# Kernel optimization log

Measured on AMD Instinct MI355X. Metric: run time of the kernel, lower is better.

The kernel has to match this reference:

```python
import jax, jax.numpy as jnp
import numpy as np

D_IN = 768
D_OUT = 768
SEQ = 2048
BATCH = 4


def setup_inputs() -> dict:
    key = jax.random.key(0)
    kx, kq, kk, kv = jax.random.split(key, 4)
    # torch Linear weight shape: [d_out, d_in]; default init ~ U(-1/sqrt(d_in), 1/sqrt(d_in))
    bound = 1.0 / np.sqrt(D_IN)
    x = jax.random.normal(kx, (BATCH, SEQ, D_IN), dtype=jnp.float32)
    Wq = jax.random.uniform(kq, (D_OUT, D_IN), jnp.float32, -bound, bound)
    Wk = jax.random.uniform(kk, (D_OUT, D_IN), jnp.float32, -bound, bound)
    Wv = jax.random.uniform(kv, (D_OUT, D_IN), jnp.float32, -bound, bound)
    return {"x": x, "Wq": Wq, "Wk": Wk, "Wv": Wv}


def reference(x, Wq, Wk, Wv):
    # QKV projections (no bias): x [b, n, d_in] @ W.T -> [b, n, d_out]
    q = jnp.einsum("bnd,od->bno", x, Wq)
    k = jnp.einsum("bnd,od->bno", x, Wk)
    v = jnp.einsum("bnd,od->bno", x, Wv)
    n = x.shape[1]
    d_k = k.shape[-1]
    # scores [b, n, n]; causal mask: positions j > i set to -inf
    scores = jnp.einsum("bqd,bkd->bqk", q, k)
    causal = jnp.triu(jnp.ones((n, n), dtype=bool), k=1)  # True above diagonal
    scores = jnp.where(causal[None, :, :], -jnp.inf, scores)
    attn = jax.nn.softmax(scores / jnp.sqrt(jnp.asarray(d_k, scores.dtype)), axis=-1)
    # dropout p=0.0 -> identity
    context = jnp.einsum("bqk,bkd->bqd", attn, v)
    return context
```

## Files before the change

### kernel.cpp

```cpp
#include <hip/hip_runtime.h>
#include <hip/hip_bf16.h>

typedef float f32x4 __attribute__((ext_vector_type(4)));
typedef short s16x8 __attribute__((ext_vector_type(8)));

#define B_ 4
#define S_ 2048
#define D_ 768

typedef const __attribute__((address_space(1))) char* gas_t;
typedef __attribute__((address_space(3))) char* las_t;

__device__ __forceinline__ void gload_lds16(const void* g, void* l) {
  __builtin_amdgcn_global_load_lds((gas_t)g, (las_t)l, 16, 0, 0);
}

__global__ void cvt_kernel(const float* __restrict__ x,
                           const float* __restrict__ wq,
                           const float* __restrict__ wk,
                           const float* __restrict__ wv,
                           __hip_bfloat16* __restrict__ xb,
                           __hip_bfloat16* __restrict__ wqb,
                           __hip_bfloat16* __restrict__ wkb,
                           __hip_bfloat16* __restrict__ wvb) {
  const int NX = B_ * S_ * D_ / 4;
  const int NW = D_ * D_ / 4;
  int stride = gridDim.x * blockDim.x;
  for (int j = blockIdx.x * blockDim.x + threadIdx.x; j < NX + 3 * NW; j += stride) {
    const float4* src; __hip_bfloat16* dst; int off;
    if (j < NX)             { src = (const float4*)x;  dst = xb;  off = j; }
    else if (j < NX + NW)   { src = (const float4*)wq; dst = wqb; off = j - NX; }
    else if (j < NX + 2*NW) { src = (const float4*)wk; dst = wkb; off = j - NX - NW; }
    else                    { src = (const float4*)wv; dst = wvb; off = j - NX - 2*NW; }
    float4 v = src[off];
    dst[4*off+0] = __float2bfloat16(v.x);
    dst[4*off+1] = __float2bfloat16(v.y);
    dst[4*off+2] = __float2bfloat16(v.z);
    dst[4*off+3] = __float2bfloat16(v.w);
  }
}

__device__ __forceinline__ void stage_tile64(const __hip_bfloat16* __restrict__ base,
                                             size_t stride, int r0, int k0,
                                             char* lds, int w, int l) {
#pragma unroll
  for (int it = 0; it < 4; ++it) {
    int ra = it * 32 + w * 8 + (l >> 3);
    int slot = (l & 7) ^ ((l >> 3) & 7);
    gload_lds16(base + (size_t)(r0 + ra) * stride + k0 + slot * 8,
                lds + it * 4096 + w * 1024);
  }
}

#define SWZ_IDX(R, s) ((R) * 64 + (((s) ^ ((R) & 7)) * 8))

__launch_bounds__(256, 2)
__global__ void qkv_gemm(const __hip_bfloat16* __restrict__ xb,
                         const __hip_bfloat16* __restrict__ wqb,
                         const __hip_bfloat16* __restrict__ wkb,
                         const __hip_bfloat16* __restrict__ wvb,
                         __hip_bfloat16* __restrict__ Qb,
                         __hip_bfloat16* __restrict__ Kb,
                         __hip_bfloat16* __restrict__ Vt) {
  __shared__ __hip_bfloat16 At[2][128 * 64];
  __shared__ __hip_bfloat16 Bt[2][128 * 64];
  const int z = blockIdx.z;
  const __hip_bfloat16* Ag;
  const __hip_bfloat16* Bg;
  int m0, n0;
  if (z == 0)      { Ag = xb;  Bg = wqb; m0 = blockIdx.x * 128; n0 = blockIdx.y * 128; }
  else if (z == 1) { Ag = xb;  Bg = wkb; m0 = blockIdx.x * 128; n0 = blockIdx.y * 128; }
  else             { Ag = wvb; Bg = xb;  m0 = blockIdx.y * 128; n0 = blockIdx.x * 128; }

  const int tid = threadIdx.x, w = tid >> 6, l = tid & 63;
  const int wr = w >> 1, wc = w & 1;
  f32x4 acc[4][4] = {};

  stage_tile64(Ag, 768, m0, 0, (char*)At[0], w, l);
  stage_tile64(Bg, 768, n0, 0, (char*)Bt[0], w, l);
  int cur = 0;
  for (int k0 = 0; k0 < 768; k0 += 64) {
    __syncthreads();
    if (k0 + 64 < 768) {
      stage_tile64(Ag, 768, m0, k0 + 64, (char*)At[cur ^ 1], w, l);
      stage_tile64(Bg, 768, n0, k0 + 64, (char*)Bt[cur ^ 1], w, l);
    }
#pragma unroll
    for (int kk = 0; kk < 2; ++kk) {
      s16x8 a[4], b[4];
      int s = kk * 4 + (l >> 4);
#pragma unroll
      for (int i = 0; i < 4; ++i) {
        int Ra = wr * 64 + i * 16 + (l & 15);
        int Rb = wc * 64 + i * 16 + (l & 15);
        a[i] = *(const s16x8*)&At[cur][SWZ_IDX(Ra, s)];
        b[i] = *(const s16x8*)&Bt[cur][SWZ_IDX(Rb, s)];
      }
#pragma unroll
      for (int i = 0; i < 4; ++i)
#pragma unroll
        for (int j = 0; j < 4; ++j)
          acc[i][j] = __builtin_amdgcn_mfma_f32_16x16x32_bf16(a[i], b[j], acc[i][j], 0, 0, 0);
    }
    cur ^= 1;
  }

  if (z < 2) {
    __hip_bfloat16* outp = (z == 0) ? Qb : Kb;
#pragma unroll
    for (int i = 0; i < 4; ++i) {
      int m = m0 + wr * 64 + i * 16 + (l >> 4) * 4;
#pragma unroll
      for (int j = 0; j < 4; ++j) {
        int n = n0 + wc * 64 + j * 16 + (l & 15);
#pragma unroll
        for (int r = 0; r < 4; ++r)
          outp[(size_t)(m + r) * 768 + n] = __float2bfloat16(acc[i][j][r]);
      }
    }
  } else {
#pragma unroll
    for (int i = 0; i < 4; ++i) {
      int dd = m0 + wr * 64 + i * 16 + (l >> 4) * 4;
#pragma unroll
      for (int j = 0; j < 4; ++j) {
        int sg = n0 + wc * 64 + j * 16 + (l & 15);
        int bb = sg >> 11, sl = sg & 2047;
#pragma unroll
        for (int r = 0; r < 4; ++r)
          Vt[(size_t)bb * D_ * S_ + (size_t)(dd + r) * S_ + sl] = __float2bfloat16(acc[i][j][r]);
      }
    }
  }
}

__launch_bounds__(256, 2)
__global__ void qk_gemm(const __hip_bfloat16* __restrict__ Qb,
                        const __hip_bfloat16* __restrict__ Kb,
                        __hip_bfloat16* __restrict__ Sb) {
  __shared__ __hip_bfloat16 At[2][128 * 64];
  __shared__ __hip_bfloat16 Bt[2][128 * 64];
  const int qt = blockIdx.x, kt = blockIdx.y, b = blockIdx.z;
  if (kt > qt) return;
  const int m0 = qt * 128, n0 = kt * 128;
  const __hip_bfloat16* Ag = Qb + (size_t)b * S_ * D_;
  const __hip_bfloat16* Bg = Kb + (size_t)b * S_ * D_;
  const int tid = threadIdx.x, w = tid >> 6, l = tid & 63;
  const int wr = w >> 1, wc = w & 1;
  const float SC = 0.03608439182435161f * 1.4426950408889634f;
  f32x4 acc[4][4] = {};

  stage_tile64(Ag, D_, m0, 0, (char*)At[0], w, l);
  stage_tile64(Bg, D_, n0, 0, (char*)Bt[0], w, l);
  int cur = 0;
  for (int k0 = 0; k0 < D_; k0 += 64) {
    __syncthreads();
    if (k0 + 64 < D_) {
      stage_tile64(Ag, D_, m0, k0 + 64, (char*)At[cur ^ 1], w, l);
      stage_tile64(Bg, D_, n0, k0 + 64, (char*)Bt[cur ^ 1], w, l);
    }
#pragma unroll
    for (int kk = 0; kk < 2; ++kk) {
      s16x8 a[4], bfr[4];
      int s = kk * 4 + (l >> 4);
#pragma unroll
      for (int i = 0; i < 4; ++i) {
        int Ra = wr * 64 + i * 16 + (l & 15);
        int Rb = wc * 64 + i * 16 + (l & 15);
        a[i]   = *(const s16x8*)&At[cur][SWZ_IDX(Ra, s)];
        bfr[i] = *(const s16x8*)&Bt[cur][SWZ_IDX(Rb, s)];
      }
#pragma unroll
      for (int i = 0; i < 4; ++i)
#pragma unroll
        for (int j = 0; j < 4; ++j)
          acc[i][j] = __builtin_amdgcn_mfma_f32_16x16x32_bf16(a[i], bfr[j], acc[i][j], 0, 0, 0);
    }
    cur ^= 1;
  }

#pragma unroll
  for (int i = 0; i < 4; ++i) {
    int m = m0 + wr * 64 + i * 16 + (l >> 4) * 4;
#pragma unroll
    for (int j = 0; j < 4; ++j) {
      int n = n0 + wc * 64 + j * 16 + (l & 15);
#pragma unroll
      for (int r = 0; r < 4; ++r) {
        float zz = (n > m + r) ? -1e30f : acc[i][j][r] * SC;
        Sb[(size_t)(b * S_ + m + r) * S_ + n] = __float2bfloat16(zz);
      }
    }
  }
}

__launch_bounds__(256, 4)
__global__ void softmax_kernel(const __hip_bfloat16* __restrict__ Sb,
                               __hip_bfloat16* __restrict__ Pb) {
  const int tid = threadIdx.x, w = tid >> 6, l = tid & 63;
  const int r = blockIdx.x * 4 + w;
  const int q = r & (S_ - 1);
  const int L = ((q >> 7) + 1) << 7;
  const ushort* srow = (const ushort*)(Sb + (size_t)r * S_);
  ushort* prow = (ushort*)(Pb + (size_t)r * S_);
  f32x4 ch[8];
#pragma unroll
  for (int it = 0; it < 8; ++it) {
    int idx = it * 256 + l * 4;
    if (idx < L) {
      ushort4 u = *(const ushort4*)&srow[idx];
      ch[it].x = __uint_as_float((unsigned)u.x << 16);
      ch[it].y = __uint_as_float((unsigned)u.y << 16);
      ch[it].z = __uint_as_float((unsigned)u.z << 16);
      ch[it].w = __uint_as_float((unsigned)u.w << 16);
    } else {
      ch[it].x = -1e30f; ch[it].y = -1e30f; ch[it].z = -1e30f; ch[it].w = -1e30f;
    }
  }
  float mx = -1e30f;
#pragma unroll
  for (int it = 0; it < 8; ++it)
    mx = fmaxf(mx, fmaxf(fmaxf(ch[it].x, ch[it].y), fmaxf(ch[it].z, ch[it].w)));
#pragma unroll
  for (int d = 1; d < 64; d <<= 1) mx = fmaxf(mx, __shfl_xor(mx, d, 64));
  float sum = 0.f;
#pragma unroll
  for (int it = 0; it < 8; ++it) {
    ch[it].x = exp2f(ch[it].x - mx);
    ch[it].y = exp2f(ch[it].y - mx);
    ch[it].z = exp2f(ch[it].z - mx);
    ch[it].w = exp2f(ch[it].w - mx);
    sum += (ch[it].x + ch[it].y) + (ch[it].z + ch[it].w);
  }
#pragma unroll
  for (int d = 1; d < 64; d <<= 1) sum += __shfl_xor(sum, d, 64);
  const float rinv = 1.0f / sum;
#pragma unroll
  for (int it = 0; it < 8; ++it) {
    int idx = it * 256 + l * 4;
    if (idx < L) {
      __hip_bfloat16 h0 = __float2bfloat16(ch[it].x * rinv);
      __hip_bfloat16 h1 = __float2bfloat16(ch[it].y * rinv);
      __hip_bfloat16 h2 = __float2bfloat16(ch[it].z * rinv);
      __hip_bfloat16 h3 = __float2bfloat16(ch[it].w * rinv);
      ushort4 u;
      u.x = *(ushort*)&h0; u.y = *(ushort*)&h1; u.z = *(ushort*)&h2; u.w = *(ushort*)&h3;
      *(ushort4*)&prow[idx] = u;
    }
  }
}

__launch_bounds__(256, 2)
__global__ void pv_gemm(const __hip_bfloat16* __restrict__ Pb,
                        const __hip_bfloat16* __restrict__ Vt,
                        float* __restrict__ out) {
  __shared__ __hip_bfloat16 At[2][128 * 64];
  __shared__ __hip_bfloat16 Bt[2][128 * 64];
  const int qt = 15 - (int)blockIdx.x, dt = blockIdx.y, b = blockIdx.z;
  const int m0 = qt * 128, n0 = dt * 128;
  const __hip_bfloat16* Ag = Pb + (size_t)b * S_ * S_;
  const __hip_bfloat16* Bg = Vt + (size_t)b * D_ * S_;
  const int tid = threadIdx.x, w = tid >> 6, l = tid & 63;
  const int wr = w >> 1, wc = w & 1;
  const int kmax = (qt + 1) * 128;
  f32x4 acc[4][4] = {};

  stage_tile64(Ag, S_, m0, 0, (char*)At[0], w, l);
  stage_tile64(Bg, S_, n0, 0, (char*)Bt[0], w, l);
  int cur = 0;
  for (int k0 = 0; k0 < kmax; k0 += 64) {
    __syncthreads();
    if (k0 + 64 < kmax) {
      stage_tile64(Ag, S_, m0, k0 + 64, (char*)At[cur ^ 1], w, l);
      stage_tile64(Bg, S_, n0, k0 + 64, (char*)Bt[cur ^ 1], w, l);
    }
#pragma unroll
    for (int kk = 0; kk < 2; ++kk) {
      s16x8 a[4], bfr[4];
      int s = kk * 4 + (l >> 4);
#pragma unroll
      for (int i = 0; i < 4; ++i) {
        int Ra = wr * 64 + i * 16 + (l & 15);
        int Rb = wc * 64 + i * 16 + (l & 15);
        a[i]   = *(const s16x8*)&At[cur][SWZ_IDX(Ra, s)];
        bfr[i] = *(const s16x8*)&Bt[cur][SWZ_IDX(Rb, s)];
      }
#pragma unroll
      for (int i = 0; i < 4; ++i)
#pragma unroll
        for (int j = 0; j < 4; ++j)
          acc[i][j] = __builtin_amdgcn_mfma_f32_16x16x32_bf16(a[i], bfr[j], acc[i][j], 0, 0, 0);
    }
    cur ^= 1;
  }

#pragma unroll
  for (int i = 0; i < 4; ++i) {
    int m = m0 + wr * 64 + i * 16 + (l >> 4) * 4;
#pragma unroll
    for (int j = 0; j < 4; ++j) {
      int n = n0 + wc * 64 + j * 16 + (l & 15);
#pragma unroll
      for (int r = 0; r < 4; ++r)
        out[(size_t)(b * S_ + m + r) * D_ + n] = acc[i][j][r];
    }
  }
}

extern "C" void kernel_launch(void* const* d_in, const int* in_sizes, int n_in,
                              void* d_out, int out_size, void* d_ws, size_t ws_size,
                              hipStream_t stream) {
  const float* x  = (const float*)d_in[0];
  const float* wq = (const float*)d_in[1];
  const float* wk = (const float*)d_in[2];
  const float* wv = (const float*)d_in[3];
  char* ws = (char*)d_ws;
  __hip_bfloat16* xb  = (__hip_bfloat16*)(ws + 0);
  __hip_bfloat16* wqb = (__hip_bfloat16*)(ws + 12582912);
  __hip_bfloat16* wkb = (__hip_bfloat16*)(ws + 12582912 + 1179648);
  __hip_bfloat16* wvb = (__hip_bfloat16*)(ws + 12582912 + 2 * 1179648);
  __hip_bfloat16* Qb  = (__hip_bfloat16*)(ws + 16121856);
  __hip_bfloat16* Kb  = (__hip_bfloat16*)(ws + 28704768);
  __hip_bfloat16* Vt  = (__hip_bfloat16*)(ws + 41287680);
  __hip_bfloat16* Sb  = (__hip_bfloat16*)(ws + 53870592);
  __hip_bfloat16* Pb  = (__hip_bfloat16*)(ws + 0);

  cvt_kernel<<<2048, 256, 0, stream>>>(x, wq, wk, wv, xb, wqb, wkb, wvb);
  qkv_gemm<<<dim3(64, 6, 3), 256, 0, stream>>>(xb, wqb, wkb, wvb, Qb, Kb, Vt);
  qk_gemm<<<dim3(16, 16, 4), 256, 0, stream>>>(Qb, Kb, Sb);
  softmax_kernel<<<2048, 256, 0, stream>>>(Sb, Pb);
  pv_gemm<<<dim3(16, 6, 4), 256, 0, stream>>>(Pb, Vt, (float*)d_out);
}
```

Baseline: 196.4 us.

## Use 256x256 tiles for QKV GEMM and split-K the long causal PV rows

The QKV projection GEMM moves to 256x256 tiles with 512 threads, explicit waitcnt/barrier scheduling and raised MFMA priority, so each block reuses more of what it loads. The PV GEMM splits the upper eight query tiles along K into two halves written to fp32 partial buffers, which evens out causal load imbalance across blocks. A new combine kernel then sums the partials into the output. This costs an extra kernel launch and extra fp32 traffic, and the larger QKV tile lowers occupancy and leaves fewer blocks (288).

After: 214.4 us. 1.09x slower.

```diff
diff --git a/kernel.cpp b/kernel.cpp
--- a/kernel.cpp
+++ b/kernel.cpp
@@ -52,83 +52,110 @@
   }
 }
 
+__device__ __forceinline__ void stage_tile256(const __hip_bfloat16* __restrict__ base,
+                                              size_t stride, int r0, int k0,
+                                              char* lds, int w, int l) {
+#pragma unroll
+  for (int it = 0; it < 4; ++it) {
+    int row = it * 64 + w * 8 + (l >> 3);
+    int slot = (l & 7) ^ ((l >> 3) & 7);
+    gload_lds16(base + (size_t)(r0 + row) * stride + k0 + slot * 8,
+                lds + it * 8192 + w * 1024);
+  }
+}
+
 #define SWZ_IDX(R, s) ((R) * 64 + (((s) ^ ((R) & 7)) * 8))
 
-__launch_bounds__(256, 2)
-__global__ void qkv_gemm(const __hip_bfloat16* __restrict__ xb,
-                         const __hip_bfloat16* __restrict__ wqb,
-                         const __hip_bfloat16* __restrict__ wkb,
-                         const __hip_bfloat16* __restrict__ wvb,
-                         __hip_bfloat16* __restrict__ Qb,
-                         __hip_bfloat16* __restrict__ Kb,
-                         __hip_bfloat16* __restrict__ Vt) {
-  __shared__ __hip_bfloat16 At[2][128 * 64];
-  __shared__ __hip_bfloat16 Bt[2][128 * 64];
+__launch_bounds__(512, 1)
+__global__ void qkv_gemm256(const __hip_bfloat16* __restrict__ xb,
+                            const __hip_bfloat16* __restrict__ wqb,
+                            const __hip_bfloat16* __restrict__ wkb,
+                            const __hip_bfloat16* __restrict__ wvb,
+                            __hip_bfloat16* __restrict__ Qb,
+                            __hip_bfloat16* __restrict__ Kb,
+                            __hip_bfloat16* __restrict__ Vt) {
+  __shared__ __hip_bfloat16 At[2][256 * 64];
+  __shared__ __hip_bfloat16 Bt[2][256 * 64];
   const int z = blockIdx.z;
   const __hip_bfloat16* Ag;
   const __hip_bfloat16* Bg;
   int m0, n0;
-  if (z == 0)      { Ag = xb;  Bg = wqb; m0 = blockIdx.x * 128; n0 = blockIdx.y * 128; }
-  else if (z == 1) { Ag = xb;  Bg = wkb; m0 = blockIdx.x * 128; n0 = blockIdx.y * 128; }
-  else             { Ag = wvb; Bg = xb;  m0 = blockIdx.y * 128; n0 = blockIdx.x * 128; }
+  if (z == 0)      { Ag = xb;  Bg = wqb; m0 = blockIdx.x * 256; n0 = blockIdx.y * 256; }
+  else if (z == 1) { Ag = xb;  Bg = wkb; m0 = blockIdx.x * 256; n0 = blockIdx.y * 256; }
+  else             { Ag = wvb; Bg = xb;  m0 = blockIdx.y * 256; n0 = blockIdx.x * 256; }
 
   const int tid = threadIdx.x, w = tid >> 6, l = tid & 63;
-  const int wr = w >> 1, wc = w & 1;
-  f32x4 acc[4][4] = {};
-
-  stage_tile64(Ag, 768, m0, 0, (char*)At[0], w, l);
-  stage_tile64(Bg, 768, n0, 0, (char*)Bt[0], w, l);
-  int cur = 0;
-  for (int k0 = 0; k0 < 768; k0 += 64) {
-    __syncthreads();
-    if (k0 + 64 < 768) {
-      stage_tile64(Ag, 768, m0, k0 + 64, (char*)At[cur ^ 1], w, l);
-      stage_tile64(Bg, 768, n0, k0 + 64, (char*)Bt[cur ^ 1], w, l);
-    }
+  const int wm = w >> 2, wn = w & 3;
+  f32x4 acc[8][4] = {};
+
+  stage_tile256(Ag, 768, m0, 0, (char*)At[0], w, l);
+  stage_tile256(Bg, 768, n0, 0, (char*)Bt[0], w, l);
+
+  const int NT = 12;
+  for (int t = 0; t < NT; ++t) {
+    __builtin_amdgcn_sched_barrier(0);
+    asm volatile("s_waitcnt lgkmcnt(0)" ::: "memory");
+    __builtin_amdgcn_s_barrier();
+    __builtin_amdgcn_sched_barrier(0);
+    if (t + 1 < NT) {
+      stage_tile256(Ag, 768, m0, (t + 1) * 64, (char*)At[(t + 1) & 1], w, l);
+      stage_tile256(Bg, 768, n0, (t + 1) * 64, (char*)Bt[(t + 1) & 1], w, l);
+      asm volatile("s_waitcnt vmcnt(8)" ::: "memory");
+    } else {
+      asm volatile("s_waitcnt vmcnt(0)" ::: "memory");
+    }
+    __builtin_amdgcn_s_barrier();
+    __builtin_amdgcn_sched_barrier(0);
+    const __hip_bfloat16* Ab = At[t & 1];
+    const __hip_bfloat16* Bb = Bt[t & 1];
 #pragma unroll
     for (int kk = 0; kk < 2; ++kk) {
-      s16x8 a[4], b[4];
+      s16x8 a[8], bfr[4];
       int s = kk * 4 + (l >> 4);
 #pragma unroll
-      for (int i = 0; i < 4; ++i) {
-        int Ra = wr * 64 + i * 16 + (l & 15);
-        int Rb = wc * 64 + i * 16 + (l & 15);
-        a[i] = *(const s16x8*)&At[cur][SWZ_IDX(Ra, s)];
-        b[i] = *(const s16x8*)&Bt[cur][SWZ_IDX(Rb, s)];
-      }
-#pragma unroll
-      for (int i = 0; i < 4; ++i)
-#pragma unroll
-        for (int j = 0; j < 4; ++j)
-          acc[i][j] = __builtin_amdgcn_mfma_f32_16x16x32_bf16(a[i], b[j], acc[i][j], 0, 0, 0);
-    }
-    cur ^= 1;
+      for (int mf = 0; mf < 8; ++mf) {
+        int R = wm * 128 + mf * 16 + (l & 15);
+        a[mf] = *(const s16x8*)&Ab[SWZ_IDX(R, s)];
+      }
+#pragma unroll
+      for (int nf = 0; nf < 4; ++nf) {
+        int R = wn * 64 + nf * 16 + (l & 15);
+        bfr[nf] = *(const s16x8*)&Bb[SWZ_IDX(R, s)];
+      }
+      __builtin_amdgcn_s_setprio(1);
+#pragma unroll
+      for (int mf = 0; mf < 8; ++mf)
+#pragma unroll
+        for (int nf = 0; nf < 4; ++nf)
+          acc[mf][nf] = __builtin_amdgcn_mfma_f32_16x16x32_bf16(a[mf], bfr[nf], acc[mf][nf], 0, 0, 0);
+      __builtin_amdgcn_s_setprio(0);
+    }
   }
 
   if (z < 2) {
     __hip_bfloat16* outp = (z == 0) ? Qb : Kb;
 #pragma unroll
-    for (int i = 0; i < 4; ++i) {
-      int m = m0 + wr * 64 + i * 16 + (l >> 4) * 4;
-#pragma unroll
-      for (int j = 0; j < 4; ++j) {
-        int n = n0 + wc * 64 + j * 16 + (l & 15);
+    for (int mf = 0; mf < 8; ++mf) {
+      int m = m0 + wm * 128 + mf * 16 + (l >> 4) * 4;
+#pragma unroll
+      for (int nf = 0; nf < 4; ++nf) {
+        int n = n0 + wn * 64 + nf * 16 + (l & 15);
 #pragma unroll
         for (int r = 0; r < 4; ++r)
-          outp[(size_t)(m + r) * 768 + n] = __float2bfloat16(acc[i][j][r]);
+          outp[(size_t)(m + r) * 768 + n] = __float2bfloat16(acc[mf][nf][r]);
       }
     }
   } else {
 #pragma unroll
-    for (int i = 0; i < 4; ++i) {
-      int dd = m0 + wr * 64 + i * 16 + (l >> 4) * 4;
-#pragma unroll
-      for (int j = 0; j < 4; ++j) {
-        int sg = n0 + wc * 64 + j * 16 + (l & 15);
+    for (int mf = 0; mf < 8; ++mf) {
+      int dd = m0 + wm * 128 + mf * 16 + (l >> 4) * 4;
+#pragma unroll
+      for (int nf = 0; nf < 4; ++nf) {
+        int sg = n0 + wn * 64 + nf * 16 + (l & 15);
         int bb = sg >> 11, sl = sg & 2047;
 #pragma unroll
         for (int r = 0; r < 4; ++r)
-          Vt[(size_t)bb * D_ * S_ + (size_t)(dd + r) * S_ + sl] = __float2bfloat16(acc[i][j][r]);
+          Vt[(size_t)bb * D_ * S_ + (size_t)(dd + r) * S_ + sl] = __float2bfloat16(acc[mf][nf][r]);
       }
     }
   }
@@ -253,24 +280,38 @@
 __launch_bounds__(256, 2)
 __global__ void pv_gemm(const __hip_bfloat16* __restrict__ Pb,
                         const __hip_bfloat16* __restrict__ Vt,
-                        float* __restrict__ out) {
+                        float* __restrict__ out,
+                        float* __restrict__ part0,
+                        float* __restrict__ part1) {
   __shared__ __hip_bfloat16 At[2][128 * 64];
   __shared__ __hip_bfloat16 Bt[2][128 * 64];
-  const int qt = 15 - (int)blockIdx.x, dt = blockIdx.y, b = blockIdx.z;
+  const int xx = 23 - (int)blockIdx.x, dt = blockIdx.y, b = blockIdx.z;
+  int qt, klo, khi;
+  float* dst; int mbase;
+  if (xx < 8) {
+    qt = xx; klo = 0; khi = (qt + 1) * 128;
+    dst = out + (size_t)b * S_ * D_; mbase = qt * 128;
+  } else {
+    int idx = xx - 8;
+    qt = 8 + (idx >> 1);
+    int half = idx & 1, kh = (qt + 1) * 64;
+    klo = half * kh; khi = klo + kh;
+    dst = (half ? part1 : part0) + (size_t)b * 1024 * D_;
+    mbase = qt * 128 - 1024;
+  }
   const int m0 = qt * 128, n0 = dt * 128;
   const __hip_bfloat16* Ag = Pb + (size_t)b * S_ * S_;
   const __hip_bfloat16* Bg = Vt + (size_t)b * D_ * S_;
   const int tid = threadIdx.x, w = tid >> 6, l = tid & 63;
   const int wr = w >> 1, wc = w & 1;
-  const int kmax = (qt + 1) * 128;
   f32x4 acc[4][4] = {};
 
-  stage_tile64(Ag, S_, m0, 0, (char*)At[0], w, l);
-  stage_tile64(Bg, S_, n0, 0, (char*)Bt[0], w, l);
+  stage_tile64(Ag, S_, m0, klo, (char*)At[0], w, l);
+  stage_tile64(Bg, S_, n0, klo, (char*)Bt[0], w, l);
   int cur = 0;
-  for (int k0 = 0; k0 < kmax; k0 += 64) {
+  for (int k0 = klo; k0 < khi; k0 += 64) {
     __syncthreads();
-    if (k0 + 64 < kmax) {
+    if (k0 + 64 < khi) {
       stage_tile64(Ag, S_, m0, k0 + 64, (char*)At[cur ^ 1], w, l);
       stage_tile64(Bg, S_, n0, k0 + 64, (char*)Bt[cur ^ 1], w, l);
     }
@@ -296,14 +337,31 @@
 
 #pragma unroll
   for (int i = 0; i < 4; ++i) {
-    int m = m0 + wr * 64 + i * 16 + (l >> 4) * 4;
+    int m = mbase + wr * 64 + i * 16 + (l >> 4) * 4;
 #pragma unroll
     for (int j = 0; j < 4; ++j) {
       int n = n0 + wc * 64 + j * 16 + (l & 15);
 #pragma unroll
       for (int r = 0; r < 4; ++r)
-        out[(size_t)(b * S_ + m + r) * D_ + n] = acc[i][j][r];
-    }
+        dst[(size_t)(m + r) * D_ + n] = acc[i][j][r];
+    }
+  }
+}
+
+__global__ void combine_kernel(const float* __restrict__ part0,
+                               const float* __restrict__ part1,
+                               float* __restrict__ out) {
+  const int N4 = B_ * 1024 * D_ / 4;
+  const float4* p0 = (const float4*)part0;
+  const float4* p1 = (const float4*)part1;
+  float4* o = (float4*)out;
+  int stride = gridDim.x * blockDim.x;
+  for (int f = blockIdx.x * blockDim.x + threadIdx.x; f < N4; f += stride) {
+    int b = f / (1024 * D_ / 4);
+    int oidx = f % (1024 * D_ / 4);
+    float4 a = p0[f], c = p1[f];
+    float4 v = make_float4(a.x + c.x, a.y + c.y, a.z + c.z, a.w + c.w);
+    o[(size_t)b * S_ * D_ / 4 + (size_t)1024 * D_ / 4 + oidx] = v;
   }
 }
 
@@ -324,10 +382,13 @@
   __hip_bfloat16* Vt  = (__hip_bfloat16*)(ws + 41287680);
   __hip_bfloat16* Sb  = (__hip_bfloat16*)(ws + 53870592);
   __hip_bfloat16* Pb  = (__hip_bfloat16*)(ws + 0);
+  float* part0 = (float*)(ws + 53870592);
+  float* part1 = (float*)(ws + 53870592 + 12582912);
 
   cvt_kernel<<<2048, 256, 0, stream>>>(x, wq, wk, wv, xb, wqb, wkb, wvb);
-  qkv_gemm<<<dim3(64, 6, 3), 256, 0, stream>>>(xb, wqb, wkb, wvb, Qb, Kb, Vt);
+  qkv_gemm256<<<dim3(32, 3, 3), 512, 0, stream>>>(xb, wqb, wkb, wvb, Qb, Kb, Vt);
   qk_gemm<<<dim3(16, 16, 4), 256, 0, stream>>>(Qb, Kb, Sb);
   softmax_kernel<<<2048, 256, 0, stream>>>(Sb, Pb);
-  pv_gemm<<<dim3(16, 6, 4), 256, 0, stream>>>(Pb, Vt, (float*)d_out);
-}
+  pv_gemm<<<dim3(24, 6, 4), 256, 0, stream>>>(Pb, Vt, (float*)d_out, part0, part1);
+  combine_kernel<<<1024, 256, 0, stream>>>(part0, part1, (float*)d_out);
+}
```

## Fuse softmax exponent into QK GEMM and split-K the heavy PV tiles

Applied to the files above, without the earlier changes.

Removes the standalone softmax kernel. The QK GEMM epilogue now writes exp2 of the scaled scores directly as bf16 probabilities, with no max subtraction, and stores partial row sums per tile. PV GEMM applies the 1/rowsum normalization at the end. Query tiles 8–15 are split into two K halves that write fp32 partials, and a new combine kernel adds them and normalizes. This cuts one full round trip of the score matrix and balances work across the causal triangle. The cost is numerical risk: dropping the running max can overflow for large scores, and partial buffers add extra traffic.

Result: slower. 206.0 us (+4.9%).

```diff
diff --git a/kernel.cpp b/kernel.cpp
--- a/kernel.cpp
+++ b/kernel.cpp
@@ -137,7 +137,8 @@
 __launch_bounds__(256, 2)
 __global__ void qk_gemm(const __hip_bfloat16* __restrict__ Qb,
                         const __hip_bfloat16* __restrict__ Kb,
-                        __hip_bfloat16* __restrict__ Sb) {
+                        __hip_bfloat16* __restrict__ Pb,
+                        float* __restrict__ RS) {
   __shared__ __hip_bfloat16 At[2][128 * 64];
   __shared__ __hip_bfloat16 Bt[2][128 * 64];
   const int qt = blockIdx.x, kt = blockIdx.y, b = blockIdx.z;
@@ -179,6 +180,12 @@
     cur ^= 1;
   }
 
+  float rps[4][4];
+#pragma unroll
+  for (int i = 0; i < 4; ++i)
+#pragma unroll
+    for (int r = 0; r < 4; ++r) rps[i][r] = 0.f;
+
 #pragma unroll
   for (int i = 0; i < 4; ++i) {
     int m = m0 + wr * 64 + i * 16 + (l >> 4) * 4;
@@ -187,65 +194,26 @@
       int n = n0 + wc * 64 + j * 16 + (l & 15);
 #pragma unroll
       for (int r = 0; r < 4; ++r) {
-        float zz = (n > m + r) ? -1e30f : acc[i][j][r] * SC;
-        Sb[(size_t)(b * S_ + m + r) * S_ + n] = __float2bfloat16(zz);
-      }
-    }
-  }
-}
-
-__launch_bounds__(256, 4)
-__global__ void softmax_kernel(const __hip_bfloat16* __restrict__ Sb,
-                               __hip_bfloat16* __restrict__ Pb) {
-  const int tid = threadIdx.x, w = tid >> 6, l = tid & 63;
-  const int r = blockIdx.x * 4 + w;
-  const int q = r & (S_ - 1);
-  const int L = ((q >> 7) + 1) << 7;
-  const ushort* srow = (const ushort*)(Sb + (size_t)r * S_);
-  ushort* prow = (ushort*)(Pb + (size_t)r * S_);
-  f32x4 ch[8];
-#pragma unroll
-  for (int it = 0; it < 8; ++it) {
-    int idx = it * 256 + l * 4;
-    if (idx < L) {
-      ushort4 u = *(const ushort4*)&srow[idx];
-      ch[it].x = __uint_as_float((unsigned)u.x << 16);
-      ch[it].y = __uint_as_float((unsigned)u.y << 16);
-      ch[it].z = __uint_as_float((unsigned)u.z << 16);
-      ch[it].w = __uint_as_float((unsigned)u.w << 16);
-    } else {
-      ch[it].x = -1e30f; ch[it].y = -1e30f; ch[it].z = -1e30f; ch[it].w = -1e30f;
-    }
-  }
-  float mx = -1e30f;
-#pragma unroll
-  for (int it = 0; it < 8; ++it)
-    mx = fmaxf(mx, fmaxf(fmaxf(ch[it].x, ch[it].y), fmaxf(ch[it].z, ch[it].w)));
-#pragma unroll
-  for (int d = 1; d < 64; d <<= 1) mx = fmaxf(mx, __shfl_xor(mx, d, 64));
-  float sum = 0.f;
-#pragma unroll
-  for (int it = 0; it < 8; ++it) {
-    ch[it].x = exp2f(ch[it].x - mx);
-    ch[it].y = exp2f(ch[it].y - mx);
-    ch[it].z = exp2f(ch[it].z - mx);
-    ch[it].w = exp2f(ch[it].w - mx);
-    sum += (ch[it].x + ch[it].y) + (ch[it].z + ch[it].w);
-  }
-#pragma unroll
-  for (int d = 1; d < 64; d <<= 1) sum += __shfl_xor(sum, d, 64);
-  const float rinv = 1.0f / sum;
-#pragma unroll
-  for (int it = 0; it < 8; ++it) {
-    int idx = it * 256 + l * 4;
-    if (idx < L) {
-      __hip_bfloat16 h0 = __float2bfloat16(ch[it].x * rinv);
-      __hip_bfloat16 h1 = __float2bfloat16(ch[it].y * rinv);
-      __hip_bfloat16 h2 = __float2bfloat16(ch[it].z * rinv);
-      __hip_bfloat16 h3 = __float2bfloat16(ch[it].w * rinv);
-      ushort4 u;
-      u.x = *(ushort*)&h0; u.y = *(ushort*)&h1; u.z = *(ushort*)&h2; u.w = *(ushort*)&h3;
-      *(ushort4*)&prow[idx] = u;
+        float p = (n > m + r) ? 0.f : exp2f(acc[i][j][r] * SC);
+        __hip_bfloat16 hp = __float2bfloat16(p);
+        rps[i][r] += __bfloat162float(hp);
+        Pb[(size_t)(b * S_ + m + r) * S_ + n] = hp;
+      }
+    }
+  }
+#pragma unroll
+  for (int d = 1; d < 16; d <<= 1)
+#pragma unroll
+    for (int i = 0; i < 4; ++i)
+#pragma unroll
+      for (int r = 0; r < 4; ++r) rps[i][r] += __shfl_xor(rps[i][r], d, 64);
+  if ((l & 15) == 0) {
+    float* slice = RS + (size_t)(((b * 16 + qt) * 16 + kt) * 2 + wc) * 128;
+#pragma unroll
+    for (int i = 0; i < 4; ++i) {
+      int row = wr * 64 + i * 16 + (l >> 4) * 4;
+#pragma unroll
+      for (int r = 0; r < 4; ++r) slice[row + r] = rps[i][r];
     }
   }
 }
@@ -253,24 +221,51 @@
 __launch_bounds__(256, 2)
 __global__ void pv_gemm(const __hip_bfloat16* __restrict__ Pb,
                         const __hip_bfloat16* __restrict__ Vt,
-                        float* __restrict__ out) {
+                        const float* __restrict__ RS,
+                        float* __restrict__ out,
+                        float* __restrict__ part0,
+                        float* __restrict__ part1) {
   __shared__ __hip_bfloat16 At[2][128 * 64];
   __shared__ __hip_bfloat16 Bt[2][128 * 64];
-  const int qt = 15 - (int)blockIdx.x, dt = blockIdx.y, b = blockIdx.z;
+  __shared__ float Ls[128];
+  const int xx = 23 - (int)blockIdx.x, dt = blockIdx.y, b = blockIdx.z;
+  int qt, klo, khi, mbase;
+  float* dst;
+  bool direct;
+  if (xx < 8) {
+    qt = xx; klo = 0; khi = (qt + 1) * 128;
+    dst = out + (size_t)b * S_ * D_; mbase = qt * 128; direct = true;
+  } else {
+    int idx = xx - 8;
+    qt = 8 + (idx >> 1);
+    int half = idx & 1;
+    int h0 = ((qt + 2) >> 1) * 128;
+    klo = half ? h0 : 0;
+    khi = half ? (qt + 1) * 128 : h0;
+    dst = (half ? part1 : part0) + (size_t)b * 1024 * D_;
+    mbase = qt * 128 - 1024; direct = false;
+  }
   const int m0 = qt * 128, n0 = dt * 128;
   const __hip_bfloat16* Ag = Pb + (size_t)b * S_ * S_;
   const __hip_bfloat16* Bg = Vt + (size_t)b * D_ * S_;
   const int tid = threadIdx.x, w = tid >> 6, l = tid & 63;
   const int wr = w >> 1, wc = w & 1;
-  const int kmax = (qt + 1) * 128;
   f32x4 acc[4][4] = {};
 
-  stage_tile64(Ag, S_, m0, 0, (char*)At[0], w, l);
-  stage_tile64(Bg, S_, n0, 0, (char*)Bt[0], w, l);
+  if (direct && tid < 128) {
+    float s = 0.f;
+    const float* base = RS + (size_t)(b * 16 + qt) * 16 * 256;
+    for (int kt = 0; kt <= qt; ++kt)
+      s += base[kt * 256 + tid] + base[kt * 256 + 128 + tid];
+    Ls[tid] = 1.0f / s;
+  }
+
+  stage_tile64(Ag, S_, m0, klo, (char*)At[0], w, l);
+  stage_tile64(Bg, S_, n0, klo, (char*)Bt[0], w, l);
   int cur = 0;
-  for (int k0 = 0; k0 < kmax; k0 += 64) {
+  for (int k0 = klo; k0 < khi; k0 += 64) {
     __syncthreads();
-    if (k0 + 64 < kmax) {
+    if (k0 + 64 < khi) {
       stage_tile64(Ag, S_, m0, k0 + 64, (char*)At[cur ^ 1], w, l);
       stage_tile64(Bg, S_, n0, k0 + 64, (char*)Bt[cur ^ 1], w, l);
     }
@@ -296,14 +291,52 @@
 
 #pragma unroll
   for (int i = 0; i < 4; ++i) {
-    int m = m0 + wr * 64 + i * 16 + (l >> 4) * 4;
+    int lr = wr * 64 + i * 16 + (l >> 4) * 4;
+    int m = mbase + lr;
 #pragma unroll
     for (int j = 0; j < 4; ++j) {
       int n = n0 + wc * 64 + j * 16 + (l & 15);
 #pragma unroll
-      for (int r = 0; r < 4; ++r)
-        out[(size_t)(b * S_ + m + r) * D_ + n] = acc[i][j][r];
-    }
+      for (int r = 0; r < 4; ++r) {
+        float v = acc[i][j][r];
+        if (direct) v *= Ls[lr + r];
+        dst[(size_t)(m + r) * D_ + n] = v;
+      }
+    }
+  }
+}
+
+__launch_bounds__(256, 4)
+__global__ void combine_kernel(const float* __restrict__ part0,
+                               const float* __restrict__ part1,
+                               const float* __restrict__ RS,
+                               float* __restrict__ out) {
+  __shared__ float Ls[32];
+  const int rg = blockIdx.x, b = blockIdx.y;
+  const int q0 = 1024 + rg * 32;
+  const int tid = threadIdx.x;
+  if (tid < 32) {
+    int q = q0 + tid, qt = q >> 7, row = q & 127;
+    float s = 0.f;
+    const float* base = RS + (size_t)(b * 16 + qt) * 16 * 256;
+    for (int kt = 0; kt <= qt; ++kt)
+      s += base[kt * 256 + row] + base[kt * 256 + 128 + row];
+    Ls[tid] = 1.0f / s;
+  }
+  __syncthreads();
+  const int F = 32 * (D_ / 4);
+  const float4* p0 = (const float4*)(part0 + (size_t)b * 1024 * D_);
+  const float4* p1 = (const float4*)(part1 + (size_t)b * 1024 * D_);
+  float4* o = (float4*)(out + (size_t)b * S_ * D_);
+  for (int f = tid; f < F; f += 256) {
+    int r = f / (D_ / 4), c = f % (D_ / 4);
+    int prow = (q0 - 1024) + r;
+    float4 a = p0[(size_t)prow * (D_ / 4) + c];
+    float4 d = p1[(size_t)prow * (D_ / 4) + c];
+    float sc = Ls[r];
+    float4 v = make_float4((a.x + d.x) * sc, (a.y + d.y) * sc,
+                           (a.z + d.z) * sc, (a.w + d.w) * sc);
+    o[(size_t)(q0 + r) * (D_ / 4) + c] = v;
   }
 }
 
@@ -322,12 +355,14 @@
   __hip_bfloat16* Qb  = (__hip_bfloat16*)(ws + 16121856);
   __hip_bfloat16* Kb  = (__hip_bfloat16*)(ws + 28704768);
   __hip_bfloat16* Vt  = (__hip_bfloat16*)(ws + 41287680);
-  __hip_bfloat16* Sb  = (__hip_bfloat16*)(ws + 53870592);
-  __hip_bfloat16* Pb  = (__hip_bfloat16*)(ws + 0);
+  __hip_bfloat16* Pb  = (__hip_bfloat16*)(ws + 53870592);
+  float* RS    = (float*)(ws + 0);
+  float* part0 = (float*)(ws + 1048576);
+  float* part1 = (float*)(ws + 1048576 + 12582912);
 
   cvt_kernel<<<2048, 256, 0, stream>>>(x, wq, wk, wv, xb, wqb, wkb, wvb);
   qkv_gemm<<<dim3(64, 6, 3), 256, 0, stream>>>(xb, wqb, wkb, wvb, Qb, Kb, Vt);
-  qk_gemm<<<dim3(16, 16, 4), 256, 0, stream>>>(Qb, Kb, Sb);
-  softmax_kernel<<<2048, 256, 0, stream>>>(Sb, Pb);
-  pv_gemm<<<dim3(16, 6, 4), 256, 0, stream>>>(Pb, Vt, (float*)d_out);
-}
+  qk_gemm<<<dim3(16, 16, 4), 256, 0, stream>>>(Qb, Kb, Pb, RS);
+  pv_gemm<<<dim3(24, 6, 4), 256, 0, stream>>>(Pb, Vt, RS, (float*)d_out, part0, part1);
+  combine_kernel<<<dim3(32, 4), 256, 0, stream>>>(part0, part1, RS, (float*)d_out);
+}
```
